# Kernel optimization log

Hardware: AMD Instinct MI355X
Metric: run time of the kernel (lower is better)

## Reference

```python
import jax, jax.numpy as jnp
import numpy as np
import math

EMBED_DIM = 1024
NUM_HEADS = 16
HEAD_DIM = EMBED_DIM // NUM_HEADS


def alibi_slopes(num_heads: int) -> np.ndarray:
    def slopes_pow2(n):
        start = 2.0 ** (-(2.0 ** (-(math.log2(n) - 3))))
        return [start * (start ** i) for i in range(n)]
    if math.log2(num_heads).is_integer():
        return np.array(slopes_pow2(num_heads), dtype=np.float32)
    closest = 2 ** math.floor(math.log2(num_heads))
    extra = slopes_pow2(2 * closest)[closest:]
    return np.array(slopes_pow2(closest) + extra[: num_heads - closest], dtype=np.float32)


def setup_inputs() -> dict:
    key = jax.random.key(0)
    ks = jax.random.split(key, 9)
    B, S, E = 2, 2048, EMBED_DIM
    scale = 1.0 / math.sqrt(E)
    x = jax.random.normal(ks[0], (B, S, E), dtype=jnp.float32)
    Wq = jax.random.normal(ks[1], (E, E), dtype=jnp.float32) * scale
    Wk = jax.random.normal(ks[2], (E, E), dtype=jnp.float32) * scale
    Wv = jax.random.normal(ks[3], (E, E), dtype=jnp.float32) * scale
    Wo = jax.random.normal(ks[4], (E, E), dtype=jnp.float32) * scale
    bq = jax.random.normal(ks[5], (E,), dtype=jnp.float32) * 0.01
    bk = jax.random.normal(ks[6], (E,), dtype=jnp.float32) * 0.01
    bv = jax.random.normal(ks[7], (E,), dtype=jnp.float32) * 0.01
    bo = jax.random.normal(ks[8], (E,), dtype=jnp.float32) * 0.01
    return {"x": x, "Wq": Wq, "bq": bq, "Wk": Wk, "bk": bk,
            "Wv": Wv, "bv": bv, "Wo": Wo, "bo": bo}


def reference(x, Wq, bq, Wk, bk, Wv, bv, Wo, bo):
    B, S, E = x.shape
    H, D = NUM_HEADS, HEAD_DIM
    # Linear layers (torch convention: y = x @ W.T + b)
    q = (x @ Wq.T + bq).reshape(B, S, H, D).transpose(0, 2, 1, 3)  # [B,H,S,D]
    k = (x @ Wk.T + bk).reshape(B, S, H, D).transpose(0, 2, 1, 3)
    v = (x @ Wv.T + bv).reshape(B, S, H, D).transpose(0, 2, 1, 3)

    # ALiBi bias: -slope_h * |i - j|
    slopes = jnp.asarray(alibi_slopes(H))                      # [H]
    pos = jnp.arange(S, dtype=jnp.float32)
    rel = jnp.abs(pos[None, :] - pos[:, None])                 # [S,S]
    bias = -slopes[:, None, None] * rel[None, :, :]            # [H,S,S]

    scores = jnp.einsum('bhqd,bhkd->bhqk', q, k) / math.sqrt(D)
    scores = scores + bias[None]
    causal = jnp.tril(jnp.ones((S, S), dtype=bool))            # keep lower triangle
    scores = jnp.where(causal[None, None], scores, -jnp.inf)
    probs = jax.nn.softmax(scores, axis=-1)
    out = jnp.einsum('bhqk,bhkd->bhqd', probs, v)              # [B,H,S,D]
    out = out.transpose(0, 2, 1, 3).reshape(B, S, E)
    return out @ Wo.T + bo
```

## Files before the change

kernel.cpp:

```cpp
#include <hip/hip_runtime.h>
#include <hip/hip_bf16.h>

typedef __bf16 bf16;
typedef __bf16 bf16x4 __attribute__((ext_vector_type(4)));
typedef __bf16 bf16x8 __attribute__((ext_vector_type(8)));
typedef float  f32x4  __attribute__((ext_vector_type(4)));

#define NEG_BIG (-1e30f)
#define LOG2E 1.44269504088896340736f

#define AS1(p) ((const __attribute__((address_space(1))) void*)(p))
#define AS3(p) ((__attribute__((address_space(3))) void*)(p))

__device__ __forceinline__ void stage16(const void* g, void* lds_uniform_base) {
    __builtin_amdgcn_global_load_lds(AS1(g), AS3(lds_uniform_base), 16, 0, 0);
}

__device__ __forceinline__ bf16x8 cvt8(const float* __restrict__ p) {
    bf16x8 r;
#pragma unroll
    for (int i = 0; i < 8; ++i) r[i] = (bf16)p[i];
    return r;
}

template <int CTRL>
__device__ __forceinline__ float dpp_max_step(float x) {
    int v = __builtin_bit_cast(int, x);
    int s = __builtin_amdgcn_update_dpp(v, v, CTRL, 0xF, 0xF, true);
    return fmaxf(x, __builtin_bit_cast(float, s));
}
template <int CTRL>
__device__ __forceinline__ float dpp_add_step(float x) {
    int v = __builtin_bit_cast(int, x);
    int s = __builtin_amdgcn_update_dpp(v, v, CTRL, 0xF, 0xF, true);
    return x + __builtin_bit_cast(float, s);
}
__device__ __forceinline__ float red16_max(float x) {
    x = dpp_max_step<0xB1>(x);
    x = dpp_max_step<0x4E>(x);
    x = dpp_max_step<0x141>(x);
    x = dpp_max_step<0x140>(x);
    return x;
}
__device__ __forceinline__ float red16_sum(float x) {
    x = dpp_add_step<0xB1>(x);
    x = dpp_add_step<0x4E>(x);
    x = dpp_add_step<0x141>(x);
    x = dpp_add_step<0x140>(x);
    return x;
}

#if __has_builtin(__builtin_amdgcn_exp2f)
#define EXP2F(x) __builtin_amdgcn_exp2f(x)
#else
#define EXP2F(x) exp2f(x)
#endif

__global__ __launch_bounds__(256) void conv_all(
    const float* __restrict__ x,  const float* __restrict__ wq,
    const float* __restrict__ wk, const float* __restrict__ wv,
    bf16* __restrict__ xb, bf16* __restrict__ wb)
{
    const int blk = blockIdx.x;
    const float* src; bf16* dst; size_t off;
    if (blk < 2048)      { src = x;  dst = xb;           off = (size_t)blk * 2048; }
    else if (blk < 2560) { src = wq; dst = wb;           off = (size_t)(blk - 2048) * 2048; }
    else if (blk < 3072) { src = wk; dst = wb + 1048576; off = (size_t)(blk - 2560) * 2048; }
    else                 { src = wv; dst = wb + 2097152; off = (size_t)(blk - 3072) * 2048; }
    const size_t i = off + (size_t)threadIdx.x * 8;
    *(bf16x8*)(dst + i) = cvt8(src + i);
}

__global__ __launch_bounds__(256) void qkv_gemm(
    const bf16* __restrict__ Xb, const bf16* __restrict__ Wb,
    const float* __restrict__ bq, const float* __restrict__ bk, const float* __restrict__ bv,
    bf16* __restrict__ qo, bf16* __restrict__ ko, bf16* __restrict__ vo)
{
    __shared__ alignas(16) bf16 As[128 * 32];
    __shared__ alignas(16) bf16 Bs[128 * 32];

    const int t    = threadIdx.x;
    const int lane = t & 63, w = t >> 6;
    const int quad = lane >> 4, col = lane & 15;
    const int nt = blockIdx.x;
    const int mt = blockIdx.y;
    const int region = nt >> 3;
    const int n0 = (nt & 7) * 128;
    const int m0 = mt * 128;
    const int K  = 1024;

    const bf16*  W    = Wb + (size_t)region * 1048576;
    const float* bias = region == 0 ? bq : (region == 1 ? bk : bv);

    const int wm = (w >> 1) * 64, wn = (w & 1) * 64;
    f32x4 acc[4][4] = {};

    for (int k0 = 0; k0 < K; k0 += 32) {
        __syncthreads();
#pragma unroll
        for (int i = 0; i < 2; ++i) {
            int c = i * 256 + t;
            stage16(Xb + (size_t)(m0 + (c >> 2)) * K + k0 + (c & 3) * 8,
                    As + (i * 256 + w * 64) * 8);
        }
#pragma unroll
        for (int i = 0; i < 2; ++i) {
            int c = i * 256 + t;
            stage16(W + (size_t)(n0 + (c >> 2)) * K + k0 + (c & 3) * 8,
                    Bs + (i * 256 + w * 64) * 8);
        }
        __syncthreads();

        bf16x8 a[4], b[4];
#pragma unroll
        for (int i = 0; i < 4; ++i)
            a[i] = *(const bf16x8*)(As + (wm + i * 16 + col) * 32 + quad * 8);
#pragma unroll
        for (int j = 0; j < 4; ++j)
            b[j] = *(const bf16x8*)(Bs + (wn + j * 16 + col) * 32 + quad * 8);
#pragma unroll
        for (int i = 0; i < 4; ++i)
#pragma unroll
            for (int j = 0; j < 4; ++j)
                acc[i][j] = __builtin_amdgcn_mfma_f32_16x16x32_bf16(a[i], b[j], acc[i][j], 0, 0, 0);
    }

    if (region == 2) {
#pragma unroll
        for (int i = 0; i < 4; ++i) {
            const int mbase = m0 + wm + i * 16 + quad * 4;
            const int b_ = mbase >> 11, s = mbase & 2047;
#pragma unroll
            for (int j = 0; j < 4; ++j) {
                const int n = n0 + wn + j * 16 + col;
                const float bb = bias[n];
                const int h = n >> 6, d = n & 63;
                bf16x4 pk;
#pragma unroll
                for (int r = 0; r < 4; ++r) pk[r] = (bf16)(acc[i][j][r] + bb);
                *(bf16x4*)(vo + ((size_t)(b_ * 16 + h) * 64 + d) * 2048 + s) = pk;
            }
        }
    } else {
        bf16* out = region == 0 ? qo : ko;
        const float scale = region == 0 ? (0.125f * LOG2E) : 1.0f;
#pragma unroll
        for (int i = 0; i < 4; ++i) {
            const int mbase = m0 + wm + i * 16 + quad * 4;
#pragma unroll
            for (int j = 0; j < 4; ++j) {
                const int n = n0 + wn + j * 16 + col;
                const float bb = bias[n];
                const int h = n >> 6, d = n & 63;
#pragma unroll
                for (int r = 0; r < 4; ++r) {
                    const int m  = mbase + r;
                    const int b_ = m >> 11, s = m & 2047;
                    out[(((size_t)(b_ * 16 + h)) * 2048 + s) * 64 + d] =
                        (bf16)((acc[i][j][r] + bb) * scale);
                }
            }
        }
    }
}

__global__ __launch_bounds__(256, 3) void attn_kernel(
    const bf16* __restrict__ Q, const bf16* __restrict__ Kg,
    const bf16* __restrict__ Vt, bf16* __restrict__ O)
{
    const int t    = threadIdx.x;
    const int lane = t & 63, w = t >> 6;
    const int quad = lane >> 4, col = lane & 15;
    const int bh   = blockIdx.x & 31;
    const int z    = blockIdx.x >> 5;
    const int qt   = 31 - z;
    const int b  = bh >> 4, h = bh & 15;
    const float nslope = -EXP2F(-0.5f * (float)(h + 1)) * LOG2E;

    const bf16* qp  = Q  + (size_t)bh * 2048 * 64;
    const bf16* kp  = Kg + (size_t)bh * 2048 * 64;
    const bf16* vtp = Vt + (size_t)bh * 64 * 2048;

    __shared__ alignas(16) bf16 Kbuf[2][64 * 64];
    __shared__ alignas(16) bf16 Vbuf[2][64 * 64];
    __shared__ alignas(16) bf16 Ps[4 * 16 * 72];
    bf16* Pw = Ps + w * (16 * 72);

    const int q0 = qt * 64;

    bf16x8 qa[2];
#pragma unroll
    for (int ks = 0; ks < 2; ++ks)
        qa[ks] = *(const bf16x8*)(qp + (size_t)(q0 + w * 16 + col) * 64
                                  + ks * 32 + quad * 8);

    float mrow[4], lrow[4], bi[4];
    f32x4 of[4] = {};
    const int gi0 = q0 + w * 16 + quad * 4;
#pragma unroll
    for (int r = 0; r < 4; ++r) {
        mrow[r] = NEG_BIG; lrow[r] = 0.f;
        bi[r] = nslope * (float)(gi0 + r);
    }

    {
#pragma unroll
        for (int i = 0; i < 2; ++i) {
            int c = i * 256 + t;
            int row = c >> 3, j8 = (c & 7) ^ (row & 7);
            stage16(kp + (size_t)row * 64 + j8 * 8, Kbuf[0] + (i * 256 + w * 64) * 8);
        }
#pragma unroll
        for (int i = 0; i < 2; ++i) {
            int c = i * 256 + t;
            int d = c >> 3, j8 = (c & 7) ^ (d & 7);
            stage16(vtp + (size_t)d * 2048 + j8 * 8, Vbuf[0] + (i * 256 + w * 64) * 8);
        }
    }
    __syncthreads();

    for (int kvt = 0; kvt <= qt; ++kvt) {
        const int kv0 = kvt * 64;
        const bf16* Kb = Kbuf[kvt & 1];
        const bf16* Vb = Vbuf[kvt & 1];

        if (kvt < qt) {
            bf16* Kn = Kbuf[(kvt & 1) ^ 1];
            bf16* Vn = Vbuf[(kvt & 1) ^ 1];
            const int nv0 = kv0 + 64;
#pragma unroll
            for (int i = 0; i < 2; ++i) {
                int c = i * 256 + t;
                int row = c >> 3, j8 = (c & 7) ^ (row & 7);
                stage16(kp + (size_t)(nv0 + row) * 64 + j8 * 8, Kn + (i * 256 + w * 64) * 8);
            }
#pragma unroll
            for (int i = 0; i < 2; ++i) {
                int c = i * 256 + t;
                int d = c >> 3, j8 = (c & 7) ^ (d & 7);
                stage16(vtp + (size_t)d * 2048 + nv0 + j8 * 8, Vn + (i * 256 + w * 64) * 8);
            }
        }

        f32x4 sc[4];
#pragma unroll
        for (int nj = 0; nj < 4; ++nj) {
            const int row = nj * 16 + col;
            const bf16* kb = Kb + row * 64;
            const int rx = row & 7;
            bf16x8 k0f = *(const bf16x8*)(kb + (quad ^ rx) * 8);
            bf16x8 k1f = *(const bf16x8*)(kb + ((quad + 4) ^ rx) * 8);
            f32x4 zz = {};
            zz = __builtin_amdgcn_mfma_f32_16x16x32_bf16(qa[0], k0f, zz, 0, 0, 0);
            zz = __builtin_amdgcn_mfma_f32_16x16x32_bf16(qa[1], k1f, zz, 0, 0, 0);
            sc[nj] = zz;
        }

        const bool diag = (kvt == qt);
        float bj[4];
#pragma unroll
        for (int nj = 0; nj < 4; ++nj)
            bj[nj] = nslope * (float)(kv0 + nj * 16 + col);

#pragma unroll
        for (int r = 0; r < 4; ++r) {
#pragma unroll
            for (int nj = 0; nj < 4; ++nj)
                sc[nj][r] += bi[r] - bj[nj];
            if (diag) {
                const int gi = gi0 + r;
#pragma unroll
                for (int nj = 0; nj < 4; ++nj)
                    if (kv0 + nj * 16 + col > gi) sc[nj][r] = NEG_BIG;
            }
            float mx = sc[0][r];
#pragma unroll
            for (int nj = 1; nj < 4; ++nj) mx = fmaxf(mx, sc[nj][r]);
            mx = red16_max(mx);
            const float mo = mrow[r];
            const float mn = fmaxf(mo, mx);
            const float alpha = EXP2F(mo - mn);
            float rs = 0.f;
#pragma unroll
            for (int nj = 0; nj < 4; ++nj) {
                float p = EXP2F(sc[nj][r] - mn);
                sc[nj][r] = p;
                rs += p;
            }
            rs = red16_sum(rs);
            mrow[r] = mn;
            lrow[r] = lrow[r] * alpha + rs;
#pragma unroll
            for (int jd = 0; jd < 4; ++jd) of[jd][r] *= alpha;
        }

#pragma unroll
        for (int nj = 0; nj < 4; ++nj)
#pragma unroll
            for (int r = 0; r < 4; ++r)
                Pw[(quad * 4 + r) * 72 + nj * 16 + col] = (bf16)sc[nj][r];

#pragma unroll
        for (int kk = 0; kk < 2; ++kk) {
            bf16x8 pa = *(const bf16x8*)(Pw + col * 72 + kk * 32 + quad * 8);
#pragma unroll
            for (int jd = 0; jd < 4; ++jd) {
                const int rd = jd * 16 + col;
                bf16x8 vbf = *(const bf16x8*)(Vb + rd * 64 + (((kk * 4 + quad) ^ (rd & 7)) * 8));
                of[jd] = __builtin_amdgcn_mfma_f32_16x16x32_bf16(pa, vbf, of[jd], 0, 0, 0);
            }
        }

        __syncthreads();
    }

#pragma unroll
    for (int r = 0; r < 4; ++r) {
        const int s = q0 + w * 16 + quad * 4 + r;
        const float inv_l = 1.f / lrow[r];
#pragma unroll
        for (int jd = 0; jd < 4; ++jd) {
            const int e = h * 64 + jd * 16 + col;
            O[((size_t)(b * 2048 + s)) * 1024 + e] = (bf16)(of[jd][r] * inv_l);
        }
    }
}

__global__ __launch_bounds__(256) void out_gemm(
    const bf16* __restrict__ A, const float* __restrict__ W,
    const float* __restrict__ bias, float* __restrict__ out)
{
    __shared__ alignas(16) bf16 As[128 * 32];
    __shared__ alignas(16) bf16 Bs[128 * 32];

    const int t    = threadIdx.x;
    const int lane = t & 63, w = t >> 6;
    const int quad = lane >> 4, col = lane & 15;
    const int n0 = blockIdx.x * 128;
    const int m0 = blockIdx.y * 128;
    const int K  = 1024;
    const int wm = (w >> 1) * 64, wn = (w & 1) * 64;
    const int r0 = t >> 2, c8 = (t & 3) * 8;
    f32x4 acc[4][4] = {};

    for (int k0 = 0; k0 < K; k0 += 32) {
        bf16x8 bx0 = cvt8(W + (size_t)(n0 + r0)      * K + k0 + c8);
        bf16x8 bx1 = cvt8(W + (size_t)(n0 + 64 + r0) * K + k0 + c8);
        __syncthreads();
#pragma unroll
        for (int i = 0; i < 2; ++i) {
            int c = i * 256 + t;
            stage16(A + (size_t)(m0 + (c >> 2)) * K + k0 + (c & 3) * 8,
                    As + (i * 256 + w * 64) * 8);
        }
        *(bf16x8*)(Bs + r0 * 32 + c8)        = bx0;
        *(bf16x8*)(Bs + (64 + r0) * 32 + c8) = bx1;
        __syncthreads();

        bf16x8 a[4], b[4];
#pragma unroll
        for (int i = 0; i < 4; ++i)
            a[i] = *(const bf16x8*)(As + (wm + i * 16 + col) * 32 + quad * 8);
#pragma unroll
        for (int j = 0; j < 4; ++j)
            b[j] = *(const bf16x8*)(Bs + (wn + j * 16 + col) * 32 + quad * 8);
#pragma unroll
        for (int i = 0; i < 4; ++i)
#pragma unroll
            for (int j = 0; j < 4; ++j)
                acc[i][j] = __builtin_amdgcn_mfma_f32_16x16x32_bf16(a[i], b[j], acc[i][j], 0, 0, 0);
    }

#pragma unroll
    for (int i = 0; i < 4; ++i) {
        const int mbase = m0 + wm + i * 16 + quad * 4;
#pragma unroll
        for (int j = 0; j < 4; ++j) {
            const int n = n0 + wn + j * 16 + col;
            const float bb = bias[n];
#pragma unroll
            for (int r = 0; r < 4; ++r)
                out[(size_t)(mbase + r) * 1024 + n] = acc[i][j][r] + bb;
        }
    }
}

extern "C" void kernel_launch(void* const* d_in, const int* in_sizes, int n_in,
                              void* d_out, int out_size, void* d_ws, size_t ws_size,
                              hipStream_t stream) {
    const float* x  = (const float*)d_in[0];
    const float* Wq = (const float*)d_in[1];
    const float* bq = (const float*)d_in[2];
    const float* Wk = (const float*)d_in[3];
    const float* bk = (const float*)d_in[4];
    const float* Wv = (const float*)d_in[5];
    const float* bv = (const float*)d_in[6];
    const float* Wo = (const float*)d_in[7];
    const float* bo = (const float*)d_in[8];
    float* out = (float*)d_out;

    bf16* xb  = (bf16*)d_ws;
    bf16* qws = xb  + 4194304;
    bf16* kws = qws + 4194304;
    bf16* vws = kws + 4194304;
    bf16* aws = xb;

    bf16* wb = (bf16*)d_out;

    conv_all<<<dim3(3584), 256, 0, stream>>>(x, Wq, Wk, Wv, xb, wb);
    qkv_gemm<<<dim3(24, 32), 256, 0, stream>>>(xb, wb, bq, bk, bv, qws, kws, vws);
    attn_kernel<<<dim3(1024), 256, 0, stream>>>(qws, kws, vws, aws);
    out_gemm<<<dim3(8, 32), 256, 0, stream>>>(aws, Wo, bo, out);
}
```

Baseline: 204.1 us.

## Load V fragments directly from global into registers and rebalance causal tile schedule

Drops the LDS double buffer for V. Each wave now loads its V^T MFMA fragments straight from global memory into registers at the start of every KV iteration, which frees LDS and lets launch bounds rise from 3 to 4 blocks per CU. The block-to-query-tile mapping changes to group tiles by head and interleave long and short causal rows (31-g, g, 15-g, 16+g) for better load balance. In exchange, every wave issues redundant global V loads with no LDS reuse across the four waves. Those loads are also not prefetched ahead of use, so their latency may be exposed before the PV MFMAs.

```diff
diff --git a/kernel.cpp b/kernel.cpp
--- a/kernel.cpp
+++ b/kernel.cpp
@@ -164,16 +164,17 @@
     }
 }
 
-__global__ __launch_bounds__(256, 3) void attn_kernel(
+__global__ __launch_bounds__(256, 4) void attn_kernel(
     const bf16* __restrict__ Q, const bf16* __restrict__ Kg,
     const bf16* __restrict__ Vt, bf16* __restrict__ O)
 {
     const int t    = threadIdx.x;
     const int lane = t & 63, w = t >> 6;
     const int quad = lane >> 4, col = lane & 15;
-    const int bh   = blockIdx.x & 31;
-    const int z    = blockIdx.x >> 5;
-    const int qt   = 31 - z;
+    const int cuid = blockIdx.x & 255;
+    const int s_   = blockIdx.x >> 8;
+    const int bh   = cuid >> 3, g = cuid & 7;
+    const int qt   = (s_ == 0) ? (31 - g) : (s_ == 1) ? g : (s_ == 2) ? (15 - g) : (16 + g);
     const int b  = bh >> 4, h = bh & 15;
     const float nslope = -EXP2F(-0.5f * (float)(h + 1)) * LOG2E;
 
@@ -182,7 +183,6 @@
     const bf16* vtp = Vt + (size_t)bh * 64 * 2048;
 
     __shared__ alignas(16) bf16 Kbuf[2][64 * 64];
-    __shared__ alignas(16) bf16 Vbuf[2][64 * 64];
     __shared__ alignas(16) bf16 Ps[4 * 16 * 72];
     bf16* Pw = Ps + w * (16 * 72);
 
@@ -210,35 +210,29 @@
             int row = c >> 3, j8 = (c & 7) ^ (row & 7);
             stage16(kp + (size_t)row * 64 + j8 * 8, Kbuf[0] + (i * 256 + w * 64) * 8);
         }
-#pragma unroll
-        for (int i = 0; i < 2; ++i) {
-            int c = i * 256 + t;
-            int d = c >> 3, j8 = (c & 7) ^ (d & 7);
-            stage16(vtp + (size_t)d * 2048 + j8 * 8, Vbuf[0] + (i * 256 + w * 64) * 8);
-        }
     }
     __syncthreads();
 
     for (int kvt = 0; kvt <= qt; ++kvt) {
         const int kv0 = kvt * 64;
         const bf16* Kb = Kbuf[kvt & 1];
-        const bf16* Vb = Vbuf[kvt & 1];
+
+        bf16x8 vc[2][4];
+#pragma unroll
+        for (int kk = 0; kk < 2; ++kk)
+#pragma unroll
+            for (int jd = 0; jd < 4; ++jd)
+                vc[kk][jd] = *(const bf16x8*)(vtp + (size_t)(jd * 16 + col) * 2048
+                                              + kv0 + kk * 32 + quad * 8);
 
         if (kvt < qt) {
             bf16* Kn = Kbuf[(kvt & 1) ^ 1];
-            bf16* Vn = Vbuf[(kvt & 1) ^ 1];
             const int nv0 = kv0 + 64;
 #pragma unroll
             for (int i = 0; i < 2; ++i) {
                 int c = i * 256 + t;
                 int row = c >> 3, j8 = (c & 7) ^ (row & 7);
                 stage16(kp + (size_t)(nv0 + row) * 64 + j8 * 8, Kn + (i * 256 + w * 64) * 8);
-            }
-#pragma unroll
-            for (int i = 0; i < 2; ++i) {
-                int c = i * 256 + t;
-                int d = c >> 3, j8 = (c & 7) ^ (d & 7);
-                stage16(vtp + (size_t)d * 2048 + nv0 + j8 * 8, Vn + (i * 256 + w * 64) * 8);
             }
         }
 
@@ -304,11 +298,8 @@
         for (int kk = 0; kk < 2; ++kk) {
             bf16x8 pa = *(const bf16x8*)(Pw + col * 72 + kk * 32 + quad * 8);
 #pragma unroll
-            for (int jd = 0; jd < 4; ++jd) {
-                const int rd = jd * 16 + col;
-                bf16x8 vbf = *(const bf16x8*)(Vb + rd * 64 + (((kk * 4 + quad) ^ (rd & 7)) * 8));
-                of[jd] = __builtin_amdgcn_mfma_f32_16x16x32_bf16(pa, vbf, of[jd], 0, 0, 0);
-            }
+            for (int jd = 0; jd < 4; ++jd)
+                of[jd] = __builtin_amdgcn_mfma_f32_16x16x32_bf16(pa, vc[kk][jd], of[jd], 0, 0, 0);
         }
 
         __syncthreads();
```

Result: slower. 251.7 us (+23.3%).

## Split long causal attention query tiles across KV ranges with a merge pass

Applied to the files above, without the earlier changes.

Query tiles 16-31 are now split into two KV-range partitions each, driven by a static partition table, so the attention grid grows from 1024 to 1536 blocks with more even work per block. The split partials are written as normalized bf16 outputs plus row max/sum, and a new merge kernel combines them using log-sum-exp weights. Launch bounds also go from 3 to 4 blocks per CU. The aim is to cut the load-imbalance tail of the causal triangle, at the cost of an extra kernel launch, partial-output traffic and extra bf16 rounding in the merge.

```diff
diff --git a/kernel.cpp b/kernel.cpp
--- a/kernel.cpp
+++ b/kernel.cpp
@@ -55,6 +55,20 @@
 #else
 #define EXP2F(x) exp2f(x)
 #endif
+
+__device__ const int4 PART_TAB[48] = {
+    {31, 0,16,30},{31,16,16,31},{30, 0,16,28},{15, 0,16,-1},
+    {30,16,15,29},{29, 0,15,26},{29,15,15,27},{28, 0,15,24},{14, 0,15,-1},
+    {28,15,14,25},{27, 0,14,22},{27,14,14,23},{26, 0,14,20},{13, 0,14,-1},
+    {26,14,13,21},{25, 0,13,18},{25,13,13,19},{24, 0,13,16},{12, 0,13,-1},
+    {24,13,12,17},{23, 0,12,14},{23,12,12,15},{22, 0,12,12},{11, 0,12,-1},
+    {22,12,11,13},{21, 0,11,10},{21,11,11,11},{20, 0,11, 8},{10, 0,11,-1},
+    {20,11,10, 9},{19, 0,10, 6},{19,10,10, 7},{18, 0,10, 4},{ 9, 0,10,-1},
+    {18,10, 9, 5},{17, 0, 9, 2},{17, 9, 9, 3},{16, 0, 9, 0},{ 8, 0, 9,-1},
+    {16, 9, 8, 1},
+    { 7, 0, 8,-1},{ 6, 0, 7,-1},{ 5, 0, 6,-1},{ 4, 0, 5,-1},
+    { 3, 0, 4,-1},{ 2, 0, 3,-1},{ 1, 0, 2,-1},{ 0, 0, 1,-1}
+};
 
 __global__ __launch_bounds__(256) void conv_all(
     const float* __restrict__ x,  const float* __restrict__ wq,
@@ -164,16 +178,18 @@
     }
 }
 
-__global__ __launch_bounds__(256, 3) void attn_kernel(
+__global__ __launch_bounds__(256, 4) void attn_kernel(
     const bf16* __restrict__ Q, const bf16* __restrict__ Kg,
-    const bf16* __restrict__ Vt, bf16* __restrict__ O)
+    const bf16* __restrict__ Vt, bf16* __restrict__ O,
+    bf16* __restrict__ Opart, float2* __restrict__ ML)
 {
     const int t    = threadIdx.x;
     const int lane = t & 63, w = t >> 6;
     const int quad = lane >> 4, col = lane & 15;
     const int bh   = blockIdx.x & 31;
-    const int z    = blockIdx.x >> 5;
-    const int qt   = 31 - z;
+    const int pe   = blockIdx.x >> 5;
+    const int4 ent = PART_TAB[pe];
+    const int qt = ent.x, kvb = ent.y, kstop = ent.y + ent.z, ps = ent.w;
     const int b  = bh >> 4, h = bh & 15;
     const float nslope = -EXP2F(-0.5f * (float)(h + 1)) * LOG2E;
 
@@ -204,29 +220,31 @@
     }
 
     {
+        const int v0 = kvb * 64;
 #pragma unroll
         for (int i = 0; i < 2; ++i) {
             int c = i * 256 + t;
             int row = c >> 3, j8 = (c & 7) ^ (row & 7);
-            stage16(kp + (size_t)row * 64 + j8 * 8, Kbuf[0] + (i * 256 + w * 64) * 8);
+            stage16(kp + (size_t)(v0 + row) * 64 + j8 * 8, Kbuf[0] + (i * 256 + w * 64) * 8);
         }
 #pragma unroll
         for (int i = 0; i < 2; ++i) {
             int c = i * 256 + t;
             int d = c >> 3, j8 = (c & 7) ^ (d & 7);
-            stage16(vtp + (size_t)d * 2048 + j8 * 8, Vbuf[0] + (i * 256 + w * 64) * 8);
+            stage16(vtp + (size_t)d * 2048 + v0 + j8 * 8, Vbuf[0] + (i * 256 + w * 64) * 8);
         }
     }
     __syncthreads();
 
-    for (int kvt = 0; kvt <= qt; ++kvt) {
+    for (int kvt = kvb; kvt < kstop; ++kvt) {
         const int kv0 = kvt * 64;
-        const bf16* Kb = Kbuf[kvt & 1];
-        const bf16* Vb = Vbuf[kvt & 1];
-
-        if (kvt < qt) {
-            bf16* Kn = Kbuf[(kvt & 1) ^ 1];
-            bf16* Vn = Vbuf[(kvt & 1) ^ 1];
+        const int pb  = (kvt - kvb) & 1;
+        const bf16* Kb = Kbuf[pb];
+        const bf16* Vb = Vbuf[pb];
+
+        if (kvt + 1 < kstop) {
+            bf16* Kn = Kbuf[pb ^ 1];
+            bf16* Vn = Vbuf[pb ^ 1];
             const int nv0 = kv0 + 64;
 #pragma unroll
             for (int i = 0; i < 2; ++i) {
@@ -314,15 +332,64 @@
         __syncthreads();
     }
 
-#pragma unroll
-    for (int r = 0; r < 4; ++r) {
-        const int s = q0 + w * 16 + quad * 4 + r;
-        const float inv_l = 1.f / lrow[r];
-#pragma unroll
-        for (int jd = 0; jd < 4; ++jd) {
-            const int e = h * 64 + jd * 16 + col;
-            O[((size_t)(b * 2048 + s)) * 1024 + e] = (bf16)(of[jd][r] * inv_l);
-        }
+    if (ps < 0) {
+#pragma unroll
+        for (int r = 0; r < 4; ++r) {
+            const int s = q0 + w * 16 + quad * 4 + r;
+            const float inv_l = 1.f / lrow[r];
+#pragma unroll
+            for (int jd = 0; jd < 4; ++jd) {
+                const int e = h * 64 + jd * 16 + col;
+                O[((size_t)(b * 2048 + s)) * 1024 + e] = (bf16)(of[jd][r] * inv_l);
+            }
+        }
+    } else {
+        const size_t base = ((size_t)(bh * 32 + ps)) * 64;
+#pragma unroll
+        for (int r = 0; r < 4; ++r) {
+            const int row = w * 16 + quad * 4 + r;
+            const float inv_l = 1.f / lrow[r];
+#pragma unroll
+            for (int jd = 0; jd < 4; ++jd)
+                Opart[(base + row) * 64 + jd * 16 + col] = (bf16)(of[jd][r] * inv_l);
+            if (col == 0)
+                ML[base + row] = make_float2(mrow[r], lrow[r]);
+        }
+    }
+}
+
+__global__ __launch_bounds__(256) void merge_kernel(
+    const bf16* __restrict__ Opart, const float2* __restrict__ ML,
+    bf16* __restrict__ O)
+{
+    const int bh = blockIdx.x & 31;
+    const int qt = 16 + (blockIdx.x >> 5);
+    const int b = bh >> 4, h = bh & 15;
+    const int p0 = (qt - 16) * 2, p1 = p0 + 1;
+    const int t = threadIdx.x;
+    const int row = t >> 2, d0 = (t & 3) * 16;
+
+    const float2 ml0 = ML[(size_t)(bh * 32 + p0) * 64 + row];
+    const float2 ml1 = ML[(size_t)(bh * 32 + p1) * 64 + row];
+    const float mt = fmaxf(ml0.x, ml1.x);
+    float w0 = ml0.y * EXP2F(ml0.x - mt);
+    float w1 = ml1.y * EXP2F(ml1.x - mt);
+    const float inv = 1.f / (w0 + w1);
+    w0 *= inv; w1 *= inv;
+
+    const bf16* a = Opart + ((size_t)(bh * 32 + p0) * 64 + row) * 64 + d0;
+    const bf16* c = Opart + ((size_t)(bh * 32 + p1) * 64 + row) * 64 + d0;
+    bf16* o = O + ((size_t)(b * 2048 + qt * 64 + row)) * 1024 + h * 64 + d0;
+
+#pragma unroll
+    for (int i = 0; i < 2; ++i) {
+        bf16x8 va = *(const bf16x8*)(a + i * 8);
+        bf16x8 vc = *(const bf16x8*)(c + i * 8);
+        bf16x8 vo;
+#pragma unroll
+        for (int e = 0; e < 8; ++e)
+            vo[e] = (bf16)((float)va[e] * w0 + (float)vc[e] * w1);
+        *(bf16x8*)(o + i * 8) = vo;
     }
 }
 
@@ -405,10 +472,13 @@
     bf16* vws = kws + 4194304;
     bf16* aws = xb;
 
-    bf16* wb = (bf16*)d_out;
+    bf16*   wb    = (bf16*)d_out;
+    bf16*   opart = (bf16*)d_out;
+    float2* ml    = (float2*)((char*)d_out + 8u * 1024 * 1024);
 
     conv_all<<<dim3(3584), 256, 0, stream>>>(x, Wq, Wk, Wv, xb, wb);
     qkv_gemm<<<dim3(24, 32), 256, 0, stream>>>(xb, wb, bq, bk, bv, qws, kws, vws);
-    attn_kernel<<<dim3(1024), 256, 0, stream>>>(qws, kws, vws, aws);
+    attn_kernel<<<dim3(1536), 256, 0, stream>>>(qws, kws, vws, aws, opart, ml);
+    merge_kernel<<<dim3(512), 256, 0, stream>>>(opart, ml, aws);
     out_gemm<<<dim3(8, 32), 256, 0, stream>>>(aws, Wo, bo, out);
 }
```

Result: slower. 213.2 us (+4.4%).
